# Kernel optimization log

Hardware: AMD Instinct MI355X
Metric: run time of the kernel (lower is better)

The kernel has to match this reference:

```python
import jax, jax.numpy as jnp
import numpy as np

N = 50000
E = 800000
IN_DIM = 128
HEADS = 4
OUT_DIM = 32
LEAKY_ALPHA = 0.4
BN_EPS = 1e-5


def setup_inputs() -> dict:
    key = jax.random.key(0)
    k_x, k_e, k_w, k_as, k_at = jax.random.split(key, 5)
    x = jax.random.normal(k_x, (N, IN_DIM), dtype=jnp.float32)
    edge_index = jax.random.randint(k_e, (2, E), 0, N, dtype=jnp.int32)
    # Linear weight stored as (in_dim, heads*out_dim) so that h = x @ W
    w_bound = 1.0 / np.sqrt(IN_DIM)
    W = jax.random.uniform(k_w, (IN_DIM, HEADS * OUT_DIM), dtype=jnp.float32,
                           minval=-w_bound, maxval=w_bound)
    # xavier_uniform with gain=1.414 on (heads, out_dim)
    xav = 1.414 * np.sqrt(6.0 / (HEADS + OUT_DIM))
    a_src = jax.random.uniform(k_as, (HEADS, OUT_DIM), dtype=jnp.float32, minval=-xav, maxval=xav)
    a_tgt = jax.random.uniform(k_at, (HEADS, OUT_DIM), dtype=jnp.float32, minval=-xav, maxval=xav)
    # BatchNorm affine params (fresh init: gamma=1, beta=0)
    gamma = jnp.ones((HEADS * OUT_DIM,), dtype=jnp.float32)
    beta = jnp.zeros((HEADS * OUT_DIM,), dtype=jnp.float32)
    return {"x": x, "W": W, "a_src": a_src, "a_tgt": a_tgt,
            "gamma": gamma, "beta": beta, "edge_index": edge_index}


def reference(x, W, a_src, a_tgt, gamma, beta, edge_index):
    src = edge_index[0]
    tgt = edge_index[1]
    n = x.shape[0]
    # Linear projection -> (N, H, D)
    h = (x @ W).reshape(n, HEADS, OUT_DIM)
    h_src = h[src]   # (E, H, D)
    h_tgt = h[tgt]   # (E, H, D)
    # Per-edge, per-head attention logits
    e_src = jnp.einsum('ehd,hd->eh', h_src, a_src)
    e_tgt = jnp.einsum('ehd,hd->eh', h_tgt, a_tgt)
    e = jax.nn.leaky_relu(e_src + e_tgt, negative_slope=LEAKY_ALPHA)
    # Global (per-head) max subtraction for numerical stability, as in original
    e = e - jnp.max(e, axis=0, keepdims=True)
    alpha = jnp.exp(e)  # (E, H)
    # Segment softmax denominator over target nodes
    alpha_sum = jax.ops.segment_sum(alpha, tgt, num_segments=n) + 1e-16  # (N, H)
    alpha = alpha / alpha_sum[tgt]
    # dropout is identity in eval mode
    # Weighted aggregation of source features into targets
    h_prime = h_src * alpha[:, :, None]  # (E, H, D)
    out = jax.ops.segment_sum(h_prime, tgt, num_segments=n)  # (N, H, D)
    out = out.reshape(n, HEADS * OUT_DIM)  # concat=True
    # BatchNorm1d in training mode: biased batch statistics
    mean = jnp.mean(out, axis=0)
    var = jnp.mean(jnp.square(out - mean), axis=0)
    out = (out - mean) * jax.lax.rsqrt(var + BN_EPS) * gamma + beta
    return out
```

## Files before the change

### kernel.cpp

```cpp
#include <hip/hip_runtime.h>
#include <math.h>

#define N_NODES 50000
#define E_EDGES 800000
#define IN_DIM 128
#define HEADS 4
#define OUT_DIM 32
#define HD 128
#define LEAKY 0.4f
#define BN_EPS 1e-5f

#define BSH 7
#define NB ((N_NODES + 127) >> BSH)
#define FB 196
#define FCH 4096
#define PCAP 2560
#define SRTCAP 3072
#define SCCH ((NB + 63) / 64)
#define K1B ((N_NODES + 63) / 64)
#define K2_BLOCKS 32
#define NPART 32

typedef __attribute__((ext_vector_type(8))) short short8;
typedef __attribute__((ext_vector_type(8))) unsigned short us8;
typedef __attribute__((ext_vector_type(4))) float f32x4;

__device__ __forceinline__ unsigned enc_max(float f) {
    unsigned u = __float_as_uint(f);
    return ((int)u >= 0) ? (u | 0x80000000u) : ~u;
}
__device__ __forceinline__ float dec_max(unsigned u) {
    return (u & 0x80000000u) ? __uint_as_float(u ^ 0x80000000u)
                             : __uint_as_float(~u);
}

__device__ __forceinline__ float leaky(float v) {
    return v > 0.f ? v : LEAKY * v;
}

__device__ __forceinline__ unsigned short f2bf(float f) {
    unsigned u = __float_as_uint(f);
    u = (u + 0x7FFFu + ((u >> 16) & 1u)) >> 16;
    return (unsigned short)u;
}
__device__ __forceinline__ float bf2f(unsigned short u) {
    return __uint_as_float(((unsigned)u) << 16);
}

struct FillSh { int est[FCH]; int hist[NB]; int rbase[NB]; };
union F1Sh { unsigned short Wl[32 * 64 * 8]; FillSh fl; };

__global__ __launch_bounds__(256) void f1_gemm_fill(
    const float* __restrict__ x, const float* __restrict__ W,
    const float* __restrict__ a_src, const float* __restrict__ a_tgt,
    const int* __restrict__ src, const int* __restrict__ tgt,
    int* __restrict__ bcur, int* __restrict__ ebkt,
    unsigned short* __restrict__ hb, float* __restrict__ s,
    float* __restrict__ t)
{
    __shared__ F1Sh sh;
    const int tid = threadIdx.x;

    if (blockIdx.x >= K1B) {
        int* est   = sh.fl.est;
        int* hist  = sh.fl.hist;
        int* rbase = sh.fl.rbase;
        int beg = (blockIdx.x - K1B) * FCH;
        int cnt = min(beg + FCH, E_EDGES) - beg;
        for (int i = tid; i < NB; i += 256) hist[i] = 0;
        __syncthreads();
        for (int j = tid; j < cnt; j += 256) {
            int sv = src[beg + j], tv = tgt[beg + j];
            est[j] = sv | (tv << 16);
            atomicAdd(&hist[tv >> BSH], 1);
        }
        __syncthreads();
        for (int i = tid; i < NB; i += 256) {
            int c = hist[i];
            if (c) {
                int r = atomicAdd(&bcur[i], c);
                rbase[i] = i * PCAP + min(r, PCAP);
            }
        }
        __syncthreads();
        for (int i = tid; i < NB; i += 256) hist[i] = 0;
        __syncthreads();
        for (int j = tid; j < cnt; j += 256) {
            int p  = est[j];
            int tv = (int)((unsigned)p >> 16);
            int b  = tv >> BSH;
            int off = atomicAdd(&hist[b], 1);
            int idx = rbase[b] + off;
            if (idx < (b + 1) * PCAP)
                ebkt[idx] = (p & 0xFFFF) | ((tv & 127) << 16);
        }
        return;
    }

    unsigned short* Wl = sh.Wl;
    for (int idx = tid; idx < 2048; idx += 256) {
        int l  = idx & 63;
        int f  = idx >> 6;
        int nt = f >> 2, kc = f & 3;
        int kbase = kc * 32 + ((l >> 4) << 3);
        int col   = nt * 16 + (l & 15);
        unsigned short* dst = &Wl[idx * 8];
#pragma unroll
        for (int j = 0; j < 8; j++)
            dst[j] = f2bf(W[(kbase + j) * HD + col]);
    }
    __syncthreads();

    const int wave = tid >> 6, lane = tid & 63;
    const int quad = lane >> 4, rl = lane & 15;
    const int row0 = blockIdx.x * 64 + wave * 16;
    const int crow = min(row0 + rl, N_NODES - 1);

    short8 a[4];
    const float* xp = x + (size_t)crow * IN_DIM + quad * 8;
#pragma unroll
    for (int kc = 0; kc < 4; kc++) {
        float4 v0 = *(const float4*)(xp + kc * 32);
        float4 v1 = *(const float4*)(xp + kc * 32 + 4);
        short8 av;
        av[0] = (short)f2bf(v0.x); av[1] = (short)f2bf(v0.y);
        av[2] = (short)f2bf(v0.z); av[3] = (short)f2bf(v0.w);
        av[4] = (short)f2bf(v1.x); av[5] = (short)f2bf(v1.y);
        av[6] = (short)f2bf(v1.z); av[7] = (short)f2bf(v1.w);
        a[kc] = av;
    }

    float asv[8], atv[8];
#pragma unroll
    for (int nt = 0; nt < 8; nt++) {
        asv[nt] = a_src[nt * 16 + rl];
        atv[nt] = a_tgt[nt * 16 + rl];
    }

    float ps[4][4], pt[4][4];
#pragma unroll
    for (int hh = 0; hh < 4; hh++)
#pragma unroll
        for (int r = 0; r < 4; r++) { ps[hh][r] = 0.f; pt[hh][r] = 0.f; }

#pragma unroll
    for (int nt = 0; nt < 8; nt++) {
        f32x4 acc = {0.f, 0.f, 0.f, 0.f};
#pragma unroll
        for (int kc = 0; kc < 4; kc++) {
            short8 b = *(const short8*)&Wl[((nt * 4 + kc) * 64 + lane) * 8];
            acc = __builtin_amdgcn_mfma_f32_16x16x32_bf16(a[kc], b, acc, 0, 0, 0);
        }
        const int ocol = nt * 16 + rl;
        const int hh   = nt >> 1;
#pragma unroll
        for (int r = 0; r < 4; r++) {
            int orow = row0 + quad * 4 + r;
            if (orow < N_NODES)
                hb[(size_t)orow * HD + ocol] = f2bf(acc[r]);
            ps[hh][r] = fmaf(acc[r], asv[nt], ps[hh][r]);
            pt[hh][r] = fmaf(acc[r], atv[nt], pt[hh][r]);
        }
    }

#pragma unroll
    for (int m = 1; m <= 8; m <<= 1) {
#pragma unroll
        for (int hh = 0; hh < 4; hh++)
#pragma unroll
            for (int r = 0; r < 4; r++) {
                ps[hh][r] += __shfl_xor(ps[hh][r], m, 64);
                pt[hh][r] += __shfl_xor(pt[hh][r], m, 64);
            }
    }
    if (rl == 0) {
#pragma unroll
        for (int r = 0; r < 4; r++) {
            int orow = row0 + quad * 4 + r;
            if (orow < N_NODES) {
#pragma unroll
                for (int hh = 0; hh < 4; hh++) {
                    s[orow * HEADS + hh] = ps[hh][r];
                    t[orow * HEADS + hh] = pt[hh][r];
                }
            }
        }
    }
}

struct SortSh {
    int ebl[SRTCAP]; int srt[SRTCAP]; int csc[NB + 1];
    int bins[128]; int deg_l[128]; int excl_l[128]; int cur_l[128];
    int wtot; int btot;
};
union F2Sh { SortSh so; float red[4][8]; };

__global__ __launch_bounds__(256) void f2_sort_max(
    const int* __restrict__ bcur, const int* __restrict__ ebkt,
    int* __restrict__ rowptr, unsigned short* __restrict__ esrc,
    const float* __restrict__ s, const float* __restrict__ t,
    unsigned* __restrict__ smax, unsigned* __restrict__ tmax)
{
    __shared__ F2Sh sh;
    int tid  = threadIdx.x;
    int lane = tid & 63, wv = tid >> 6;

    if (blockIdx.x >= NB) {
        int bI = blockIdx.x - NB;
        float sm0 = -INFINITY, sm1 = -INFINITY, sm2 = -INFINITY, sm3 = -INFINITY;
        float tm0 = -INFINITY, tm1 = -INFINITY, tm2 = -INFINITY, tm3 = -INFINITY;
        for (int n = bI * 256 + tid; n < N_NODES; n += K2_BLOCKS * 256) {
            float4 s4 = ((const float4*)s)[n];
            float4 t4 = ((const float4*)t)[n];
            sm0 = fmaxf(sm0, s4.x); sm1 = fmaxf(sm1, s4.y);
            sm2 = fmaxf(sm2, s4.z); sm3 = fmaxf(sm3, s4.w);
            tm0 = fmaxf(tm0, t4.x); tm1 = fmaxf(tm1, t4.y);
            tm2 = fmaxf(tm2, t4.z); tm3 = fmaxf(tm3, t4.w);
        }
#pragma unroll
        for (int m = 32; m >= 1; m >>= 1) {
            sm0 = fmaxf(sm0, __shfl_xor(sm0, m, 64));
            sm1 = fmaxf(sm1, __shfl_xor(sm1, m, 64));
            sm2 = fmaxf(sm2, __shfl_xor(sm2, m, 64));
            sm3 = fmaxf(sm3, __shfl_xor(sm3, m, 64));
            tm0 = fmaxf(tm0, __shfl_xor(tm0, m, 64));
            tm1 = fmaxf(tm1, __shfl_xor(tm1, m, 64));
            tm2 = fmaxf(tm2, __shfl_xor(tm2, m, 64));
            tm3 = fmaxf(tm3, __shfl_xor(tm3, m, 64));
        }
        if (lane == 0) {
            sh.red[wv][0] = sm0; sh.red[wv][1] = sm1;
            sh.red[wv][2] = sm2; sh.red[wv][3] = sm3;
            sh.red[wv][4] = tm0; sh.red[wv][5] = tm1;
            sh.red[wv][6] = tm2; sh.red[wv][7] = tm3;
        }
        __syncthreads();
        if (tid < 8) {
            float v = fmaxf(fmaxf(sh.red[0][tid], sh.red[1][tid]),
                            fmaxf(sh.red[2][tid], sh.red[3][tid]));
            unsigned* dst = (tid < 4) ? &smax[tid] : &tmax[tid - 4];
            atomicMax(dst, enc_max(v));
        }
        return;
    }

    int b = blockIdx.x;
    int* ebl    = sh.so.ebl;
    int* srt    = sh.so.srt;
    int* csc    = sh.so.csc;
    int* bins   = sh.so.bins;
    int* deg_l  = sh.so.deg_l;
    int* excl_l = sh.so.excl_l;
    int* cur_l  = sh.so.cur_l;

    for (int i = tid; i < NB; i += 256) csc[i] = min(bcur[i], PCAP);
    if (tid < 128) { deg_l[tid] = 0; cur_l[tid] = 0; bins[tid] = 0; }
    __syncthreads();
    if (tid < 64) {
        int cb = tid * SCCH;
        int loc[SCCH];
        int sum = 0;
#pragma unroll
        for (int k = 0; k < SCCH; k++) {
            int idx = cb + k;
            int v = (idx < NB) ? csc[idx] : 0;
            loc[k] = sum; sum += v;
        }
        int ss = sum;
#pragma unroll
        for (int off = 1; off < 64; off <<= 1) {
            int u = __shfl_up(ss, off, 64);
            if (tid >= off) ss += u;
        }
        int excl = ss - sum;
#pragma unroll
        for (int k = 0; k < SCCH; k++) {
            int idx = cb + k;
            if (idx < NB) csc[idx] = excl + loc[k];
        }
        if (tid == 63) {
            csc[NB] = excl + sum;
            if (b == 0) rowptr[N_NODES] = excl + sum;
        }
    }
    __syncthreads();
    int base_in = b * PCAP;
    int base    = csc[b];
    int cnt     = csc[b + 1] - base;

    for (int j = tid; j < cnt; j += 256) {
        int p = ebkt[base_in + j];
        ebl[j] = p;
        atomicAdd(&bins[(p & 0xFFFF) >> 9], 1);
    }
    __syncthreads();
    {
        int v = (tid < 128) ? bins[tid] : 0;
        int ssv = v;
#pragma unroll
        for (int off = 1; off < 64; off <<= 1) {
            int u = __shfl_up(ssv, off, 64);
            if (lane >= off) ssv += u;
        }
        if (tid == 63) sh.so.btot = ssv;
        __syncthreads();
        if (tid < 128) bins[tid] = ssv - v + ((wv == 1) ? sh.so.btot : 0);
        __syncthreads();
    }
    for (int j = tid; j < cnt; j += 256) {
        int p = ebl[j];
        int pos = atomicAdd(&bins[(p & 0xFFFF) >> 9], 1);
        srt[pos] = p;
    }
    __syncthreads();
    for (int j = tid; j < cnt; j += 256)
        atomicAdd(&deg_l[srt[j] >> 16], 1);
    __syncthreads();

    int v = (tid < 128) ? deg_l[tid] : 0;
    int sv2 = v;
#pragma unroll
    for (int off = 1; off < 64; off <<= 1) {
        int u = __shfl_up(sv2, off, 64);
        if (lane >= off) sv2 += u;
    }
    if (tid == 63) sh.so.wtot = sv2;
    __syncthreads();
    if (tid < 128) {
        int ex = sv2 - v + ((wv == 1) ? sh.so.wtot : 0);
        excl_l[tid] = ex;
        int node = (b << BSH) + tid;
        if (node < N_NODES) rowptr[node] = base + ex;
    }
    __syncthreads();
    for (int j = tid; j < cnt; j += 256) {
        int p  = srt[j];
        int tl = p >> 16;
        int off = atomicAdd(&cur_l[tl], 1);
        esrc[base + excl_l[tl] + off] = (unsigned short)(p & 0xFFFF);
    }
}

__global__ __launch_bounds__(256) void f3_pull_stats(
    const int* __restrict__ rowptr, const unsigned short* __restrict__ esrc,
    const float* __restrict__ s, const float* __restrict__ t,
    const unsigned* __restrict__ smax, const unsigned* __restrict__ tmax,
    const unsigned short* __restrict__ hb, unsigned short* __restrict__ outpb,
    float* __restrict__ bnsum_part, float* __restrict__ bnsq_part)
{
    __shared__ float lsum[HD], lsq[HD];
    int tid = threadIdx.x;
    if (tid < HD) { lsum[tid] = 0.f; lsq[tid] = 0.f; }
    __syncthreads();

    int g = blockIdx.x * 256 + tid;
    int node = g >> 4;
    int lane = g & 15;
    int head = lane >> 2;
    int beg = rowptr[node];
    int end = rowptr[node + 1];
    float mx = leaky(dec_max(smax[head]) + dec_max(tmax[head]));
    float tv = t[node * HEADS + head];

    float p0 = 0.f, p1 = 0.f, p2 = 0.f, p3 = 0.f;
    float p4 = 0.f, p5 = 0.f, p6 = 0.f, p7 = 0.f, psum = 0.f;
    float q0 = 0.f, q1 = 0.f, q2 = 0.f, q3 = 0.f;
    float q4 = 0.f, q5 = 0.f, q6 = 0.f, q7 = 0.f, qsum = 0.f;
    const unsigned short* hbase = hb + lane * 8;

    for (int j = beg; j < end; j += 8) {
        int lim = end - j;
        int si[8];
#pragma unroll
        for (int u = 0; u < 8; u++) {
            int uu = (u < lim) ? u : (lim - 1);
            si[u] = esrc[j + uu];
        }
        float sv[8];
        us8 hv[8];
#pragma unroll
        for (int u = 0; u < 8; u++) {
            sv[u] = s[si[u] * HEADS + head];
            hv[u] = *(const us8*)(hbase + (size_t)si[u] * HD);
        }
        float al[8];
#pragma unroll
        for (int u = 0; u < 8; u++) {
            float a = __expf(leaky(sv[u] + tv) - mx);
            al[u] = (u < lim) ? a : 0.f;
        }
#pragma unroll
        for (int u = 0; u < 8; u += 2) {
            float a0 = al[u], a1 = al[u + 1];
            p0 = fmaf(a0, bf2f(hv[u][0]), p0);  q0 = fmaf(a1, bf2f(hv[u+1][0]), q0);
            p1 = fmaf(a0, bf2f(hv[u][1]), p1);  q1 = fmaf(a1, bf2f(hv[u+1][1]), q1);
            p2 = fmaf(a0, bf2f(hv[u][2]), p2);  q2 = fmaf(a1, bf2f(hv[u+1][2]), q2);
            p3 = fmaf(a0, bf2f(hv[u][3]), p3);  q3 = fmaf(a1, bf2f(hv[u+1][3]), q3);
            p4 = fmaf(a0, bf2f(hv[u][4]), p4);  q4 = fmaf(a1, bf2f(hv[u+1][4]), q4);
            p5 = fmaf(a0, bf2f(hv[u][5]), p5);  q5 = fmaf(a1, bf2f(hv[u+1][5]), q5);
            p6 = fmaf(a0, bf2f(hv[u][6]), p6);  q6 = fmaf(a1, bf2f(hv[u+1][6]), q6);
            p7 = fmaf(a0, bf2f(hv[u][7]), p7);  q7 = fmaf(a1, bf2f(hv[u+1][7]), q7);
            psum += a0; qsum += a1;
        }
    }

    float w = 1.0f / (psum + qsum + 1e-16f);
    us8 o;
    o[0] = f2bf((p0 + q0) * w); o[1] = f2bf((p1 + q1) * w);
    o[2] = f2bf((p2 + q2) * w); o[3] = f2bf((p3 + q3) * w);
    o[4] = f2bf((p4 + q4) * w); o[5] = f2bf((p5 + q5) * w);
    o[6] = f2bf((p6 + q6) * w); o[7] = f2bf((p7 + q7) * w);
    *(us8*)(outpb + (size_t)node * HD + lane * 8) = o;

#pragma unroll
    for (int i = 0; i < 8; i++) {
        float f = bf2f(o[i]);
        atomicAdd(&lsum[lane * 8 + i], f);
        atomicAdd(&lsq[lane * 8 + i], f * f);
    }
    __syncthreads();
    if (tid < HD) {
        int ps = blockIdx.x & (NPART - 1);
        unsafeAtomicAdd(&bnsum_part[ps * HD + tid], lsum[tid]);
        unsafeAtomicAdd(&bnsq_part [ps * HD + tid], lsq[tid]);
    }
}

__global__ __launch_bounds__(256) void f4_apply(
    const unsigned short* __restrict__ outpb,
    const float* __restrict__ bnsum_part, const float* __restrict__ bnsq_part,
    const float* __restrict__ gamma, const float* __restrict__ beta,
    float* __restrict__ out)
{
    __shared__ float scs[HD], shs[HD];
    int tid = threadIdx.x;
    if (tid < HD) {
        float sm = 0.f, sq = 0.f;
#pragma unroll 4
        for (int p = 0; p < NPART; p++) {
            sm += bnsum_part[p * HD + tid];
            sq += bnsq_part [p * HD + tid];
        }
        float inv_n = 1.0f / (float)N_NODES;
        float mean = sm * inv_n;
        float var  = sq * inv_n - mean * mean;
        float sc   = gamma[tid] * rsqrtf(var + BN_EPS);
        scs[tid] = sc;
        shs[tid] = beta[tid] - mean * sc;
    }
    __syncthreads();

    int c8  = tid & 15;
    int grp = tid >> 4;
    float scale[8], shift[8];
#pragma unroll
    for (int i = 0; i < 8; i++) {
        scale[i] = scs[c8 * 8 + i];
        shift[i] = shs[c8 * 8 + i];
    }
    int base = blockIdx.x * 256;
    int end  = min(base + 256, N_NODES);
    for (int r = base + grp; r < end; r += 16) {
        us8 v = *(const us8*)(outpb + (size_t)r * HD + c8 * 8);
        float4 o0, o1;
        o0.x = fmaf(bf2f(v[0]), scale[0], shift[0]);
        o0.y = fmaf(bf2f(v[1]), scale[1], shift[1]);
        o0.z = fmaf(bf2f(v[2]), scale[2], shift[2]);
        o0.w = fmaf(bf2f(v[3]), scale[3], shift[3]);
        o1.x = fmaf(bf2f(v[4]), scale[4], shift[4]);
        o1.y = fmaf(bf2f(v[5]), scale[5], shift[5]);
        o1.z = fmaf(bf2f(v[6]), scale[6], shift[6]);
        o1.w = fmaf(bf2f(v[7]), scale[7], shift[7]);
        float* op = out + (size_t)r * HD + c8 * 8;
        ((float4*)op)[0] = o0;
        ((float4*)op)[1] = o1;
    }
}

extern "C" void kernel_launch(void* const* d_in, const int* in_sizes, int n_in,
                              void* d_out, int out_size, void* d_ws, size_t ws_size,
                              hipStream_t stream)
{
    const float* x     = (const float*)d_in[0];
    const float* W     = (const float*)d_in[1];
    const float* a_src = (const float*)d_in[2];
    const float* a_tgt = (const float*)d_in[3];
    const float* gamma = (const float*)d_in[4];
    const float* beta  = (const float*)d_in[5];
    const int*   eidx  = (const int*)d_in[6];
    const int* src = eidx;
    const int* tgt = eidx + E_EDGES;
    float* out = (float*)d_out;

    unsigned short* hb    = (unsigned short*)d_ws;
    float*          s     = (float*)d_ws + 3200000;
    float*          t     = s + (size_t)N_NODES * HEADS;
    unsigned short* outpb = (unsigned short*)(t + (size_t)N_NODES * HEADS);
    int*            ebkt  = (int*)outpb;
    unsigned short* esrc  = outpb + 6400000;
    int*            rowptr= (int*)(esrc + E_EDGES);
    int*      bcur  = rowptr + N_NODES + 1;
    unsigned* smax  = (unsigned*)(bcur + 392);
    unsigned* tmax  = smax + 4;
    float*    bnsum_part = (float*)(tmax + 4);
    float*    bnsq_part  = bnsum_part + NPART * HD;
    size_t zero_bytes = (392 + 8 + 2 * NPART * HD) * 4;
    hipMemsetAsync(bcur, 0, zero_bytes, stream);

    f1_gemm_fill<<<K1B + FB, 256, 0, stream>>>(x, W, a_src, a_tgt,
                                               src, tgt, bcur, ebkt,
                                               hb, s, t);
    f2_sort_max<<<NB + K2_BLOCKS, 256, 0, stream>>>(bcur, ebkt, rowptr, esrc,
                                                    s, t, smax, tmax);
    f3_pull_stats<<<(N_NODES * 16) / 256, 256, 0, stream>>>(
        rowptr, esrc, s, t, smax, tmax, hb, outpb, bnsum_part, bnsq_part);
    f4_apply<<<(N_NODES + 255) / 256, 256, 0, stream>>>(
        outpb, bnsum_part, bnsq_part, gamma, beta, out);
}
```

Measured before the change: 219.9 us.

## Fuse four kernels into one persistent kernel with software grid barriers

Merges the GEMM/bucket-fill, sort/max, pull-aggregation and BatchNorm stages into a single kernel of K1B+FB blocks separated by atomic-counter grid barriers. The goal is to remove three kernel-launch gaps and their tail effects. The sort step drops the secondary source-binning pass, and BN statistics are now gathered in a separate stage over contiguous row ranges. Correctness depends on all 978 blocks being co-resident, which launch_bounds(256,4) on 256 CUs should allow. The aggregation loop becomes grid-strided, and each barrier adds spin-wait latency.

```diff
diff --git a/kernel.cpp b/kernel.cpp
--- a/kernel.cpp
+++ b/kernel.cpp
@@ -15,11 +15,12 @@
 #define FB 196
 #define FCH 4096
 #define PCAP 2560
-#define SRTCAP 3072
 #define SCCH ((NB + 63) / 64)
 #define K1B ((N_NODES + 63) / 64)
 #define K2_BLOCKS 32
-#define NPART 32
+#define GRID (K1B + FB)
+#define NPART 64
+#define SROWS ((N_NODES + GRID - 1) / GRID)
 
 typedef __attribute__((ext_vector_type(8))) short short8;
 typedef __attribute__((ext_vector_type(8))) unsigned short us8;
@@ -47,25 +48,53 @@
     return __uint_as_float(((unsigned)u) << 16);
 }
 
+__device__ __forceinline__ void gridbar(int* ctr) {
+    __syncthreads();
+    if (threadIdx.x == 0) {
+        __hip_atomic_fetch_add(ctr, 1, __ATOMIC_ACQ_REL,
+                               __HIP_MEMORY_SCOPE_AGENT);
+        while (__hip_atomic_load(ctr, __ATOMIC_ACQUIRE,
+                                 __HIP_MEMORY_SCOPE_AGENT) < GRID)
+            __builtin_amdgcn_s_sleep(8);
+    }
+    __syncthreads();
+}
+
 struct FillSh { int est[FCH]; int hist[NB]; int rbase[NB]; };
-union F1Sh { unsigned short Wl[32 * 64 * 8]; FillSh fl; };
-
-__global__ __launch_bounds__(256) void f1_gemm_fill(
+struct SortSh {
+    int ebl[PCAP]; int csc[NB + 1];
+    int deg_l[128]; int excl_l[128]; int cur_l[128];
+    int wtot;
+};
+struct StatSh { float lsum[HD]; float lsq[HD]; };
+union MegaSh { unsigned short Wl[32 * 64 * 8]; FillSh fl; SortSh so;
+               StatSh st; float red[4][8]; };
+
+__global__ __launch_bounds__(256, 4) void mega(
     const float* __restrict__ x, const float* __restrict__ W,
     const float* __restrict__ a_src, const float* __restrict__ a_tgt,
     const int* __restrict__ src, const int* __restrict__ tgt,
     int* __restrict__ bcur, int* __restrict__ ebkt,
     unsigned short* __restrict__ hb, float* __restrict__ s,
-    float* __restrict__ t)
+    float* __restrict__ t, int* __restrict__ rowptr,
+    unsigned short* __restrict__ esrc,
+    unsigned* __restrict__ smax, unsigned* __restrict__ tmax,
+    unsigned short* __restrict__ outpb,
+    float* __restrict__ bnp_sum, float* __restrict__ bnp_sq,
+    float* __restrict__ gsc, float* __restrict__ gsh,
+    const float* __restrict__ gamma, const float* __restrict__ beta,
+    float* __restrict__ out, int* __restrict__ bars)
 {
-    __shared__ F1Sh sh;
-    const int tid = threadIdx.x;
-
-    if (blockIdx.x >= K1B) {
+    __shared__ MegaSh sh;
+    const int tid  = threadIdx.x;
+    const int bid  = blockIdx.x;
+    const int lane = tid & 63, wv = tid >> 6;
+
+    if (bid >= K1B) {
         int* est   = sh.fl.est;
         int* hist  = sh.fl.hist;
         int* rbase = sh.fl.rbase;
-        int beg = (blockIdx.x - K1B) * FCH;
+        int beg = (bid - K1B) * FCH;
         int cnt = min(beg + FCH, E_EDGES) - beg;
         for (int i = tid; i < NB; i += 256) hist[i] = 0;
         __syncthreads();
@@ -94,119 +123,173 @@
             if (idx < (b + 1) * PCAP)
                 ebkt[idx] = (p & 0xFFFF) | ((tv & 127) << 16);
         }
-        return;
-    }
-
-    unsigned short* Wl = sh.Wl;
-    for (int idx = tid; idx < 2048; idx += 256) {
-        int l  = idx & 63;
-        int f  = idx >> 6;
-        int nt = f >> 2, kc = f & 3;
-        int kbase = kc * 32 + ((l >> 4) << 3);
-        int col   = nt * 16 + (l & 15);
-        unsigned short* dst = &Wl[idx * 8];
-#pragma unroll
-        for (int j = 0; j < 8; j++)
-            dst[j] = f2bf(W[(kbase + j) * HD + col]);
-    }
-    __syncthreads();
-
-    const int wave = tid >> 6, lane = tid & 63;
-    const int quad = lane >> 4, rl = lane & 15;
-    const int row0 = blockIdx.x * 64 + wave * 16;
-    const int crow = min(row0 + rl, N_NODES - 1);
-
-    short8 a[4];
-    const float* xp = x + (size_t)crow * IN_DIM + quad * 8;
-#pragma unroll
-    for (int kc = 0; kc < 4; kc++) {
-        float4 v0 = *(const float4*)(xp + kc * 32);
-        float4 v1 = *(const float4*)(xp + kc * 32 + 4);
-        short8 av;
-        av[0] = (short)f2bf(v0.x); av[1] = (short)f2bf(v0.y);
-        av[2] = (short)f2bf(v0.z); av[3] = (short)f2bf(v0.w);
-        av[4] = (short)f2bf(v1.x); av[5] = (short)f2bf(v1.y);
-        av[6] = (short)f2bf(v1.z); av[7] = (short)f2bf(v1.w);
-        a[kc] = av;
-    }
-
-    float asv[8], atv[8];
-#pragma unroll
-    for (int nt = 0; nt < 8; nt++) {
-        asv[nt] = a_src[nt * 16 + rl];
-        atv[nt] = a_tgt[nt * 16 + rl];
-    }
-
-    float ps[4][4], pt[4][4];
-#pragma unroll
-    for (int hh = 0; hh < 4; hh++)
-#pragma unroll
-        for (int r = 0; r < 4; r++) { ps[hh][r] = 0.f; pt[hh][r] = 0.f; }
-
-#pragma unroll
-    for (int nt = 0; nt < 8; nt++) {
-        f32x4 acc = {0.f, 0.f, 0.f, 0.f};
+    } else {
+        unsigned short* Wl = sh.Wl;
+        for (int idx = tid; idx < 2048; idx += 256) {
+            int l  = idx & 63;
+            int f  = idx >> 6;
+            int nt = f >> 2, kc = f & 3;
+            int kbase = kc * 32 + ((l >> 4) << 3);
+            int col   = nt * 16 + (l & 15);
+            unsigned short* dst = &Wl[idx * 8];
+#pragma unroll
+            for (int j = 0; j < 8; j++)
+                dst[j] = f2bf(W[(kbase + j) * HD + col]);
+        }
+        __syncthreads();
+
+        const int quad = lane >> 4, rl = lane & 15;
+        const int row0 = bid * 64 + wv * 16;
+        const int crow = min(row0 + rl, N_NODES - 1);
+
+        short8 a[4];
+        const float* xp = x + (size_t)crow * IN_DIM + quad * 8;
 #pragma unroll
         for (int kc = 0; kc < 4; kc++) {
-            short8 b = *(const short8*)&Wl[((nt * 4 + kc) * 64 + lane) * 8];
-            acc = __builtin_amdgcn_mfma_f32_16x16x32_bf16(a[kc], b, acc, 0, 0, 0);
-        }
-        const int ocol = nt * 16 + rl;
-        const int hh   = nt >> 1;
-#pragma unroll
-        for (int r = 0; r < 4; r++) {
-            int orow = row0 + quad * 4 + r;
-            if (orow < N_NODES)
-                hb[(size_t)orow * HD + ocol] = f2bf(acc[r]);
-            ps[hh][r] = fmaf(acc[r], asv[nt], ps[hh][r]);
-            pt[hh][r] = fmaf(acc[r], atv[nt], pt[hh][r]);
-        }
-    }
-
-#pragma unroll
-    for (int m = 1; m <= 8; m <<= 1) {
+            float4 v0 = *(const float4*)(xp + kc * 32);
+            float4 v1 = *(const float4*)(xp + kc * 32 + 4);
+            short8 av;
+            av[0] = (short)f2bf(v0.x); av[1] = (short)f2bf(v0.y);
+            av[2] = (short)f2bf(v0.z); av[3] = (short)f2bf(v0.w);
+            av[4] = (short)f2bf(v1.x); av[5] = (short)f2bf(v1.y);
+            av[6] = (short)f2bf(v1.z); av[7] = (short)f2bf(v1.w);
+            a[kc] = av;
+        }
+
+        float asv[8], atv[8];
+#pragma unroll
+        for (int nt = 0; nt < 8; nt++) {
+            asv[nt] = a_src[nt * 16 + rl];
+            atv[nt] = a_tgt[nt * 16 + rl];
+        }
+
+        float ps[4][4], pt[4][4];
 #pragma unroll
         for (int hh = 0; hh < 4; hh++)
 #pragma unroll
+            for (int r = 0; r < 4; r++) { ps[hh][r] = 0.f; pt[hh][r] = 0.f; }
+
+#pragma unroll
+        for (int nt = 0; nt < 8; nt++) {
+            f32x4 acc = {0.f, 0.f, 0.f, 0.f};
+#pragma unroll
+            for (int kc = 0; kc < 4; kc++) {
+                short8 b = *(const short8*)&Wl[((nt * 4 + kc) * 64 + lane) * 8];
+                acc = __builtin_amdgcn_mfma_f32_16x16x32_bf16(a[kc], b, acc, 0, 0, 0);
+            }
+            const int ocol = nt * 16 + rl;
+            const int hh   = nt >> 1;
+#pragma unroll
             for (int r = 0; r < 4; r++) {
-                ps[hh][r] += __shfl_xor(ps[hh][r], m, 64);
-                pt[hh][r] += __shfl_xor(pt[hh][r], m, 64);
-            }
-    }
-    if (rl == 0) {
-#pragma unroll
-        for (int r = 0; r < 4; r++) {
-            int orow = row0 + quad * 4 + r;
-            if (orow < N_NODES) {
-#pragma unroll
-                for (int hh = 0; hh < 4; hh++) {
-                    s[orow * HEADS + hh] = ps[hh][r];
-                    t[orow * HEADS + hh] = pt[hh][r];
+                int orow = row0 + quad * 4 + r;
+                if (orow < N_NODES)
+                    hb[(size_t)orow * HD + ocol] = f2bf(acc[r]);
+                ps[hh][r] = fmaf(acc[r], asv[nt], ps[hh][r]);
+                pt[hh][r] = fmaf(acc[r], atv[nt], pt[hh][r]);
+            }
+        }
+
+#pragma unroll
+        for (int m = 1; m <= 8; m <<= 1) {
+#pragma unroll
+            for (int hh = 0; hh < 4; hh++)
+#pragma unroll
+                for (int r = 0; r < 4; r++) {
+                    ps[hh][r] += __shfl_xor(ps[hh][r], m, 64);
+                    pt[hh][r] += __shfl_xor(pt[hh][r], m, 64);
                 }
-            }
-        }
-    }
-}
-
-struct SortSh {
-    int ebl[SRTCAP]; int srt[SRTCAP]; int csc[NB + 1];
-    int bins[128]; int deg_l[128]; int excl_l[128]; int cur_l[128];
-    int wtot; int btot;
-};
-union F2Sh { SortSh so; float red[4][8]; };
-
-__global__ __launch_bounds__(256) void f2_sort_max(
-    const int* __restrict__ bcur, const int* __restrict__ ebkt,
-    int* __restrict__ rowptr, unsigned short* __restrict__ esrc,
-    const float* __restrict__ s, const float* __restrict__ t,
-    unsigned* __restrict__ smax, unsigned* __restrict__ tmax)
-{
-    __shared__ F2Sh sh;
-    int tid  = threadIdx.x;
-    int lane = tid & 63, wv = tid >> 6;
-
-    if (blockIdx.x >= NB) {
-        int bI = blockIdx.x - NB;
+        }
+        if (rl == 0) {
+#pragma unroll
+            for (int r = 0; r < 4; r++) {
+                int orow = row0 + quad * 4 + r;
+                if (orow < N_NODES) {
+#pragma unroll
+                    for (int hh = 0; hh < 4; hh++) {
+                        s[orow * HEADS + hh] = ps[hh][r];
+                        t[orow * HEADS + hh] = pt[hh][r];
+                    }
+                }
+            }
+        }
+    }
+
+    gridbar(&bars[0]);
+
+    if (bid < NB) {
+        int b = bid;
+        int* ebl    = sh.so.ebl;
+        int* csc    = sh.so.csc;
+        int* deg_l  = sh.so.deg_l;
+        int* excl_l = sh.so.excl_l;
+        int* cur_l  = sh.so.cur_l;
+
+        for (int i = tid; i < NB; i += 256) csc[i] = min(bcur[i], PCAP);
+        if (tid < 128) { deg_l[tid] = 0; cur_l[tid] = 0; }
+        __syncthreads();
+        if (tid < 64) {
+            int cb = tid * SCCH;
+            int loc[SCCH];
+            int sum = 0;
+#pragma unroll
+            for (int k = 0; k < SCCH; k++) {
+                int idx = cb + k;
+                int v = (idx < NB) ? csc[idx] : 0;
+                loc[k] = sum; sum += v;
+            }
+            int ss = sum;
+#pragma unroll
+            for (int off = 1; off < 64; off <<= 1) {
+                int u = __shfl_up(ss, off, 64);
+                if (tid >= off) ss += u;
+            }
+            int excl = ss - sum;
+#pragma unroll
+            for (int k = 0; k < SCCH; k++) {
+                int idx = cb + k;
+                if (idx < NB) csc[idx] = excl + loc[k];
+            }
+            if (tid == 63) {
+                csc[NB] = excl + sum;
+                if (b == 0) rowptr[N_NODES] = excl + sum;
+            }
+        }
+        __syncthreads();
+        int base_in = b * PCAP;
+        int base    = csc[b];
+        int cnt     = csc[b + 1] - base;
+
+        for (int j = tid; j < cnt; j += 256) {
+            int p = ebkt[base_in + j];
+            ebl[j] = p;
+            atomicAdd(&deg_l[p >> 16], 1);
+        }
+        __syncthreads();
+
+        int v = (tid < 128) ? deg_l[tid] : 0;
+        int sv2 = v;
+#pragma unroll
+        for (int off = 1; off < 64; off <<= 1) {
+            int u = __shfl_up(sv2, off, 64);
+            if (lane >= off) sv2 += u;
+        }
+        if (tid == 63) sh.so.wtot = sv2;
+        __syncthreads();
+        if (tid < 128) {
+            int ex = sv2 - v + ((wv == 1) ? sh.so.wtot : 0);
+            excl_l[tid] = ex;
+            int node = (b << BSH) + tid;
+            if (node < N_NODES) rowptr[node] = base + ex;
+        }
+        __syncthreads();
+        for (int j = tid; j < cnt; j += 256) {
+            int p  = ebl[j];
+            int tl = p >> 16;
+            int off = atomicAdd(&cur_l[tl], 1);
+            esrc[base + excl_l[tl] + off] = (unsigned short)(p & 0xFFFF);
+        }
+    } else if (bid < NB + K2_BLOCKS) {
+        int bI = bid - NB;
         float sm0 = -INFINITY, sm1 = -INFINITY, sm2 = -INFINITY, sm3 = -INFINITY;
         float tm0 = -INFINITY, tm1 = -INFINITY, tm2 = -INFINITY, tm3 = -INFINITY;
         for (int n = bI * 256 + tid; n < N_NODES; n += K2_BLOCKS * 256) {
@@ -241,239 +324,149 @@
             unsigned* dst = (tid < 4) ? &smax[tid] : &tmax[tid - 4];
             atomicMax(dst, enc_max(v));
         }
-        return;
-    }
-
-    int b = blockIdx.x;
-    int* ebl    = sh.so.ebl;
-    int* srt    = sh.so.srt;
-    int* csc    = sh.so.csc;
-    int* bins   = sh.so.bins;
-    int* deg_l  = sh.so.deg_l;
-    int* excl_l = sh.so.excl_l;
-    int* cur_l  = sh.so.cur_l;
-
-    for (int i = tid; i < NB; i += 256) csc[i] = min(bcur[i], PCAP);
-    if (tid < 128) { deg_l[tid] = 0; cur_l[tid] = 0; bins[tid] = 0; }
-    __syncthreads();
-    if (tid < 64) {
-        int cb = tid * SCCH;
-        int loc[SCCH];
-        int sum = 0;
-#pragma unroll
-        for (int k = 0; k < SCCH; k++) {
-            int idx = cb + k;
-            int v = (idx < NB) ? csc[idx] : 0;
-            loc[k] = sum; sum += v;
-        }
-        int ss = sum;
-#pragma unroll
-        for (int off = 1; off < 64; off <<= 1) {
-            int u = __shfl_up(ss, off, 64);
-            if (tid >= off) ss += u;
-        }
-        int excl = ss - sum;
-#pragma unroll
-        for (int k = 0; k < SCCH; k++) {
-            int idx = cb + k;
-            if (idx < NB) csc[idx] = excl + loc[k];
-        }
-        if (tid == 63) {
-            csc[NB] = excl + sum;
-            if (b == 0) rowptr[N_NODES] = excl + sum;
-        }
-    }
-    __syncthreads();
-    int base_in = b * PCAP;
-    int base    = csc[b];
-    int cnt     = csc[b + 1] - base;
-
-    for (int j = tid; j < cnt; j += 256) {
-        int p = ebkt[base_in + j];
-        ebl[j] = p;
-        atomicAdd(&bins[(p & 0xFFFF) >> 9], 1);
-    }
-    __syncthreads();
+    }
+
+    gridbar(&bars[1]);
+
+    for (int g = bid * 256 + tid; g < N_NODES * 16; g += GRID * 256) {
+        int node = g >> 4;
+        int lane16 = g & 15;
+        int head = lane16 >> 2;
+        int beg = rowptr[node];
+        int end = rowptr[node + 1];
+        float mx = leaky(dec_max(smax[head]) + dec_max(tmax[head]));
+        float tv = t[node * HEADS + head];
+
+        float p0 = 0.f, p1 = 0.f, p2 = 0.f, p3 = 0.f;
+        float p4 = 0.f, p5 = 0.f, p6 = 0.f, p7 = 0.f, psum = 0.f;
+        float q0 = 0.f, q1 = 0.f, q2 = 0.f, q3 = 0.f;
+        float q4 = 0.f, q5 = 0.f, q6 = 0.f, q7 = 0.f, qsum = 0.f;
+        const unsigned short* hbase = hb + lane16 * 8;
+
+        for (int j = beg; j < end; j += 8) {
+            int lim = end - j;
+            int si[8];
+#pragma unroll
+            for (int u = 0; u < 8; u++) {
+                int uu = (u < lim) ? u : (lim - 1);
+                si[u] = __builtin_nontemporal_load(&esrc[j + uu]);
+            }
+            float sv[8];
+            us8 hv[8];
+#pragma unroll
+            for (int u = 0; u < 8; u++) {
+                sv[u] = s[si[u] * HEADS + head];
+                hv[u] = *(const us8*)(hbase + (size_t)si[u] * HD);
+            }
+            float al[8];
+#pragma unroll
+            for (int u = 0; u < 8; u++) {
+                float a = __expf(leaky(sv[u] + tv) - mx);
+                al[u] = (u < lim) ? a : 0.f;
+            }
+#pragma unroll
+            for (int u = 0; u < 8; u += 2) {
+                float a0 = al[u], a1 = al[u + 1];
+                p0 = fmaf(a0, bf2f(hv[u][0]), p0);  q0 = fmaf(a1, bf2f(hv[u+1][0]), q0);
+                p1 = fmaf(a0, bf2f(hv[u][1]), p1);  q1 = fmaf(a1, bf2f(hv[u+1][1]), q1);
+                p2 = fmaf(a0, bf2f(hv[u][2]), p2);  q2 = fmaf(a1, bf2f(hv[u+1][2]), q2);
+                p3 = fmaf(a0, bf2f(hv[u][3]), p3);  q3 = fmaf(a1, bf2f(hv[u+1][3]), q3);
+                p4 = fmaf(a0, bf2f(hv[u][4]), p4);  q4 = fmaf(a1, bf2f(hv[u+1][4]), q4);
+                p5 = fmaf(a0, bf2f(hv[u][5]), p5);  q5 = fmaf(a1, bf2f(hv[u+1][5]), q5);
+                p6 = fmaf(a0, bf2f(hv[u][6]), p6);  q6 = fmaf(a1, bf2f(hv[u+1][6]), q6);
+                p7 = fmaf(a0, bf2f(hv[u][7]), p7);  q7 = fmaf(a1, bf2f(hv[u+1][7]), q7);
+                psum += a0; qsum += a1;
+            }
+        }
+
+        float w = 1.0f / (psum + qsum + 1e-16f);
+        us8 o;
+        o[0] = f2bf((p0 + q0) * w); o[1] = f2bf((p1 + q1) * w);
+        o[2] = f2bf((p2 + q2) * w); o[3] = f2bf((p3 + q3) * w);
+        o[4] = f2bf((p4 + q4) * w); o[5] = f2bf((p5 + q5) * w);
+        o[6] = f2bf((p6 + q6) * w); o[7] = f2bf((p7 + q7) * w);
+        *(us8*)(outpb + (size_t)node * HD + lane16 * 8) = o;
+    }
+
+    gridbar(&bars[2]);
+
     {
-        int v = (tid < 128) ? bins[tid] : 0;
-        int ssv = v;
-#pragma unroll
-        for (int off = 1; off < 64; off <<= 1) {
-            int u = __shfl_up(ssv, off, 64);
-            if (lane >= off) ssv += u;
-        }
-        if (tid == 63) sh.so.btot = ssv;
-        __syncthreads();
-        if (tid < 128) bins[tid] = ssv - v + ((wv == 1) ? sh.so.btot : 0);
-        __syncthreads();
-    }
-    for (int j = tid; j < cnt; j += 256) {
-        int p = ebl[j];
-        int pos = atomicAdd(&bins[(p & 0xFFFF) >> 9], 1);
-        srt[pos] = p;
-    }
-    __syncthreads();
-    for (int j = tid; j < cnt; j += 256)
-        atomicAdd(&deg_l[srt[j] >> 16], 1);
-    __syncthreads();
-
-    int v = (tid < 128) ? deg_l[tid] : 0;
-    int sv2 = v;
-#pragma unroll
-    for (int off = 1; off < 64; off <<= 1) {
-        int u = __shfl_up(sv2, off, 64);
-        if (lane >= off) sv2 += u;
-    }
-    if (tid == 63) sh.so.wtot = sv2;
-    __syncthreads();
-    if (tid < 128) {
-        int ex = sv2 - v + ((wv == 1) ? sh.so.wtot : 0);
-        excl_l[tid] = ex;
-        int node = (b << BSH) + tid;
-        if (node < N_NODES) rowptr[node] = base + ex;
-    }
-    __syncthreads();
-    for (int j = tid; j < cnt; j += 256) {
-        int p  = srt[j];
-        int tl = p >> 16;
-        int off = atomicAdd(&cur_l[tl], 1);
-        esrc[base + excl_l[tl] + off] = (unsigned short)(p & 0xFFFF);
-    }
-}
-
-__global__ __launch_bounds__(256) void f3_pull_stats(
-    const int* __restrict__ rowptr, const unsigned short* __restrict__ esrc,
-    const float* __restrict__ s, const float* __restrict__ t,
-    const unsigned* __restrict__ smax, const unsigned* __restrict__ tmax,
-    const unsigned short* __restrict__ hb, unsigned short* __restrict__ outpb,
-    float* __restrict__ bnsum_part, float* __restrict__ bnsq_part)
-{
-    __shared__ float lsum[HD], lsq[HD];
-    int tid = threadIdx.x;
-    if (tid < HD) { lsum[tid] = 0.f; lsq[tid] = 0.f; }
-    __syncthreads();
-
-    int g = blockIdx.x * 256 + tid;
-    int node = g >> 4;
-    int lane = g & 15;
-    int head = lane >> 2;
-    int beg = rowptr[node];
-    int end = rowptr[node + 1];
-    float mx = leaky(dec_max(smax[head]) + dec_max(tmax[head]));
-    float tv = t[node * HEADS + head];
-
-    float p0 = 0.f, p1 = 0.f, p2 = 0.f, p3 = 0.f;
-    float p4 = 0.f, p5 = 0.f, p6 = 0.f, p7 = 0.f, psum = 0.f;
-    float q0 = 0.f, q1 = 0.f, q2 = 0.f, q3 = 0.f;
-    float q4 = 0.f, q5 = 0.f, q6 = 0.f, q7 = 0.f, qsum = 0.f;
-    const unsigned short* hbase = hb + lane * 8;
-
-    for (int j = beg; j < end; j += 8) {
-        int lim = end - j;
-        int si[8];
-#pragma unroll
-        for (int u = 0; u < 8; u++) {
-            int uu = (u < lim) ? u : (lim - 1);
-            si[u] = esrc[j + uu];
-        }
-        float sv[8];
-        us8 hv[8];
-#pragma unroll
-        for (int u = 0; u < 8; u++) {
-            sv[u] = s[si[u] * HEADS + head];
-            hv[u] = *(const us8*)(hbase + (size_t)si[u] * HD);
-        }
-        float al[8];
-#pragma unroll
-        for (int u = 0; u < 8; u++) {
-            float a = __expf(leaky(sv[u] + tv) - mx);
-            al[u] = (u < lim) ? a : 0.f;
-        }
-#pragma unroll
-        for (int u = 0; u < 8; u += 2) {
-            float a0 = al[u], a1 = al[u + 1];
-            p0 = fmaf(a0, bf2f(hv[u][0]), p0);  q0 = fmaf(a1, bf2f(hv[u+1][0]), q0);
-            p1 = fmaf(a0, bf2f(hv[u][1]), p1);  q1 = fmaf(a1, bf2f(hv[u+1][1]), q1);
-            p2 = fmaf(a0, bf2f(hv[u][2]), p2);  q2 = fmaf(a1, bf2f(hv[u+1][2]), q2);
-            p3 = fmaf(a0, bf2f(hv[u][3]), p3);  q3 = fmaf(a1, bf2f(hv[u+1][3]), q3);
-            p4 = fmaf(a0, bf2f(hv[u][4]), p4);  q4 = fmaf(a1, bf2f(hv[u+1][4]), q4);
-            p5 = fmaf(a0, bf2f(hv[u][5]), p5);  q5 = fmaf(a1, bf2f(hv[u+1][5]), q5);
-            p6 = fmaf(a0, bf2f(hv[u][6]), p6);  q6 = fmaf(a1, bf2f(hv[u+1][6]), q6);
-            p7 = fmaf(a0, bf2f(hv[u][7]), p7);  q7 = fmaf(a1, bf2f(hv[u+1][7]), q7);
-            psum += a0; qsum += a1;
-        }
-    }
-
-    float w = 1.0f / (psum + qsum + 1e-16f);
-    us8 o;
-    o[0] = f2bf((p0 + q0) * w); o[1] = f2bf((p1 + q1) * w);
-    o[2] = f2bf((p2 + q2) * w); o[3] = f2bf((p3 + q3) * w);
-    o[4] = f2bf((p4 + q4) * w); o[5] = f2bf((p5 + q5) * w);
-    o[6] = f2bf((p6 + q6) * w); o[7] = f2bf((p7 + q7) * w);
-    *(us8*)(outpb + (size_t)node * HD + lane * 8) = o;
-
-#pragma unroll
-    for (int i = 0; i < 8; i++) {
-        float f = bf2f(o[i]);
-        atomicAdd(&lsum[lane * 8 + i], f);
-        atomicAdd(&lsq[lane * 8 + i], f * f);
-    }
-    __syncthreads();
-    if (tid < HD) {
-        int ps = blockIdx.x & (NPART - 1);
-        unsafeAtomicAdd(&bnsum_part[ps * HD + tid], lsum[tid]);
-        unsafeAtomicAdd(&bnsq_part [ps * HD + tid], lsq[tid]);
-    }
-}
-
-__global__ __launch_bounds__(256) void f4_apply(
-    const unsigned short* __restrict__ outpb,
-    const float* __restrict__ bnsum_part, const float* __restrict__ bnsq_part,
-    const float* __restrict__ gamma, const float* __restrict__ beta,
-    float* __restrict__ out)
-{
-    __shared__ float scs[HD], shs[HD];
-    int tid = threadIdx.x;
-    if (tid < HD) {
+        int c8  = tid & 15;
+        int grp = tid >> 4;
+        if (tid < HD) { sh.st.lsum[tid] = 0.f; sh.st.lsq[tid] = 0.f; }
+        __syncthreads();
+        int rbeg = bid * SROWS;
+        int rend = min(rbeg + SROWS, N_NODES);
+        float sm[8], sq[8];
+#pragma unroll
+        for (int i = 0; i < 8; i++) { sm[i] = 0.f; sq[i] = 0.f; }
+        for (int r = rbeg + grp; r < rend; r += 16) {
+            us8 v = *(const us8*)(outpb + (size_t)r * HD + c8 * 8);
+#pragma unroll
+            for (int i = 0; i < 8; i++) {
+                float f = bf2f(v[i]);
+                sm[i] += f;
+                sq[i] = fmaf(f, f, sq[i]);
+            }
+        }
+#pragma unroll
+        for (int i = 0; i < 8; i++) {
+            atomicAdd(&sh.st.lsum[c8 * 8 + i], sm[i]);
+            atomicAdd(&sh.st.lsq[c8 * 8 + i], sq[i]);
+        }
+        __syncthreads();
+        if (tid < HD && rbeg < N_NODES) {
+            int ps = bid & (NPART - 1);
+            unsafeAtomicAdd(&bnp_sum[ps * HD + tid], sh.st.lsum[tid]);
+            unsafeAtomicAdd(&bnp_sq [ps * HD + tid], sh.st.lsq[tid]);
+        }
+    }
+
+    gridbar(&bars[3]);
+
+    if (bid == 0 && tid < HD) {
         float sm = 0.f, sq = 0.f;
 #pragma unroll 4
         for (int p = 0; p < NPART; p++) {
-            sm += bnsum_part[p * HD + tid];
-            sq += bnsq_part [p * HD + tid];
+            sm += bnp_sum[p * HD + tid];
+            sq += bnp_sq [p * HD + tid];
         }
         float inv_n = 1.0f / (float)N_NODES;
         float mean = sm * inv_n;
         float var  = sq * inv_n - mean * mean;
         float sc   = gamma[tid] * rsqrtf(var + BN_EPS);
-        scs[tid] = sc;
-        shs[tid] = beta[tid] - mean * sc;
-    }
-    __syncthreads();
-
-    int c8  = tid & 15;
-    int grp = tid >> 4;
-    float scale[8], shift[8];
-#pragma unroll
-    for (int i = 0; i < 8; i++) {
-        scale[i] = scs[c8 * 8 + i];
-        shift[i] = shs[c8 * 8 + i];
-    }
-    int base = blockIdx.x * 256;
-    int end  = min(base + 256, N_NODES);
-    for (int r = base + grp; r < end; r += 16) {
-        us8 v = *(const us8*)(outpb + (size_t)r * HD + c8 * 8);
-        float4 o0, o1;
-        o0.x = fmaf(bf2f(v[0]), scale[0], shift[0]);
-        o0.y = fmaf(bf2f(v[1]), scale[1], shift[1]);
-        o0.z = fmaf(bf2f(v[2]), scale[2], shift[2]);
-        o0.w = fmaf(bf2f(v[3]), scale[3], shift[3]);
-        o1.x = fmaf(bf2f(v[4]), scale[4], shift[4]);
-        o1.y = fmaf(bf2f(v[5]), scale[5], shift[5]);
-        o1.z = fmaf(bf2f(v[6]), scale[6], shift[6]);
-        o1.w = fmaf(bf2f(v[7]), scale[7], shift[7]);
-        float* op = out + (size_t)r * HD + c8 * 8;
-        ((float4*)op)[0] = o0;
-        ((float4*)op)[1] = o1;
+        gsc[tid] = sc;
+        gsh[tid] = beta[tid] - mean * sc;
+    }
+
+    gridbar(&bars[4]);
+
+    {
+        int c8  = tid & 15;
+        int grp = tid >> 4;
+        float scale[8], shift[8];
+#pragma unroll
+        for (int i = 0; i < 8; i++) {
+            scale[i] = gsc[c8 * 8 + i];
+            shift[i] = gsh[c8 * 8 + i];
+        }
+        int rbeg = bid * SROWS;
+        int rend = min(rbeg + SROWS, N_NODES);
+        for (int r = rbeg + grp; r < rend; r += 16) {
+            us8 v = *(const us8*)(outpb + (size_t)r * HD + c8 * 8);
+            float4 o0, o1;
+            o0.x = fmaf(bf2f(v[0]), scale[0], shift[0]);
+            o0.y = fmaf(bf2f(v[1]), scale[1], shift[1]);
+            o0.z = fmaf(bf2f(v[2]), scale[2], shift[2]);
+            o0.w = fmaf(bf2f(v[3]), scale[3], shift[3]);
+            o1.x = fmaf(bf2f(v[4]), scale[4], shift[4]);
+            o1.y = fmaf(bf2f(v[5]), scale[5], shift[5]);
+            o1.z = fmaf(bf2f(v[6]), scale[6], shift[6]);
+            o1.w = fmaf(bf2f(v[7]), scale[7], shift[7]);
+            float* op = out + (size_t)r * HD + c8 * 8;
+            ((float4*)op)[0] = o0;
+            ((float4*)op)[1] = o1;
+        }
     }
 }
 
@@ -502,18 +495,16 @@
     int*      bcur  = rowptr + N_NODES + 1;
     unsigned* smax  = (unsigned*)(bcur + 392);
     unsigned* tmax  = smax + 4;
-    float*    bnsum_part = (float*)(tmax + 4);
-    float*    bnsq_part  = bnsum_part + NPART * HD;
-    size_t zero_bytes = (392 + 8 + 2 * NPART * HD) * 4;
+    int*      bars  = (int*)(tmax + 4);
+    float*    bnp_sum = (float*)(bars + 8);
+    float*    bnp_sq  = bnp_sum + NPART * HD;
+    size_t zero_bytes = (392 + 8 + 8 + 2 * NPART * HD) * 4;
+    float*    gsc = bnp_sq + NPART * HD;
+    float*    gsh = gsc + HD;
     hipMemsetAsync(bcur, 0, zero_bytes, stream);
 
-    f1_gemm_fill<<<K1B + FB, 256, 0, stream>>>(x, W, a_src, a_tgt,
-                                               src, tgt, bcur, ebkt,
-                                               hb, s, t);
-    f2_sort_max<<<NB + K2_BLOCKS, 256, 0, stream>>>(bcur, ebkt, rowptr, esrc,
-                                                    s, t, smax, tmax);
-    f3_pull_stats<<<(N_NODES * 16) / 256, 256, 0, stream>>>(
-        rowptr, esrc, s, t, smax, tmax, hb, outpb, bnsum_part, bnsq_part);
-    f4_apply<<<(N_NODES + 255) / 256, 256, 0, stream>>>(
-        outpb, bnsum_part, bnsq_part, gamma, beta, out);
-}
+    mega<<<GRID, 256, 0, stream>>>(x, W, a_src, a_tgt, src, tgt,
+                                   bcur, ebkt, hb, s, t, rowptr, esrc,
+                                   smax, tmax, outpb, bnp_sum, bnp_sq,
+                                   gsc, gsh, gamma, beta, out, bars);
+}
```

New measurement: 857.5 us. +290.0%, slower.

## Drop source-bin presort in bucket sort and use wave-shuffle BN partial reduction

Applied to the files above, without the earlier changes.

Removes the intermediate counting sort by source-id bins inside the per-bucket CSR build, counting degrees and scattering directly from the loaded edge list, which cuts shared memory and several barriers. In the pull kernel, the shared-memory atomic BatchNorm reduction and block barrier are replaced with xor-shuffle reductions within each wave followed by global atomics from 16 lanes. The partial-sum count is doubled to spread atomic contention, and edge source indices are read with nontemporal loads. The drop of the source presort loses source locality within each target's edge list, which may hurt gather cache behaviour, and per-wave global atomics increase atomic traffic.

```diff
diff --git a/kernel.cpp b/kernel.cpp
--- a/kernel.cpp
+++ b/kernel.cpp
@@ -15,11 +15,10 @@
 #define FB 196
 #define FCH 4096
 #define PCAP 2560
-#define SRTCAP 3072
 #define SCCH ((NB + 63) / 64)
 #define K1B ((N_NODES + 63) / 64)
 #define K2_BLOCKS 32
-#define NPART 32
+#define NPART 64
 
 typedef __attribute__((ext_vector_type(8))) short short8;
 typedef __attribute__((ext_vector_type(8))) unsigned short us8;
@@ -189,9 +188,9 @@
 }
 
 struct SortSh {
-    int ebl[SRTCAP]; int srt[SRTCAP]; int csc[NB + 1];
-    int bins[128]; int deg_l[128]; int excl_l[128]; int cur_l[128];
-    int wtot; int btot;
+    int ebl[PCAP]; int csc[NB + 1];
+    int deg_l[128]; int excl_l[128]; int cur_l[128];
+    int wtot;
 };
 union F2Sh { SortSh so; float red[4][8]; };
 
@@ -246,15 +245,13 @@
 
     int b = blockIdx.x;
     int* ebl    = sh.so.ebl;
-    int* srt    = sh.so.srt;
     int* csc    = sh.so.csc;
-    int* bins   = sh.so.bins;
     int* deg_l  = sh.so.deg_l;
     int* excl_l = sh.so.excl_l;
     int* cur_l  = sh.so.cur_l;
 
     for (int i = tid; i < NB; i += 256) csc[i] = min(bcur[i], PCAP);
-    if (tid < 128) { deg_l[tid] = 0; cur_l[tid] = 0; bins[tid] = 0; }
+    if (tid < 128) { deg_l[tid] = 0; cur_l[tid] = 0; }
     __syncthreads();
     if (tid < 64) {
         int cb = tid * SCCH;
@@ -291,30 +288,8 @@
     for (int j = tid; j < cnt; j += 256) {
         int p = ebkt[base_in + j];
         ebl[j] = p;
-        atomicAdd(&bins[(p & 0xFFFF) >> 9], 1);
-    }
-    __syncthreads();
-    {
-        int v = (tid < 128) ? bins[tid] : 0;
-        int ssv = v;
-#pragma unroll
-        for (int off = 1; off < 64; off <<= 1) {
-            int u = __shfl_up(ssv, off, 64);
-            if (lane >= off) ssv += u;
-        }
-        if (tid == 63) sh.so.btot = ssv;
-        __syncthreads();
-        if (tid < 128) bins[tid] = ssv - v + ((wv == 1) ? sh.so.btot : 0);
-        __syncthreads();
-    }
-    for (int j = tid; j < cnt; j += 256) {
-        int p = ebl[j];
-        int pos = atomicAdd(&bins[(p & 0xFFFF) >> 9], 1);
-        srt[pos] = p;
-    }
-    __syncthreads();
-    for (int j = tid; j < cnt; j += 256)
-        atomicAdd(&deg_l[srt[j] >> 16], 1);
+        atomicAdd(&deg_l[p >> 16], 1);
+    }
     __syncthreads();
 
     int v = (tid < 128) ? deg_l[tid] : 0;
@@ -334,26 +309,21 @@
     }
     __syncthreads();
     for (int j = tid; j < cnt; j += 256) {
-        int p  = srt[j];
+        int p  = ebl[j];
         int tl = p >> 16;
         int off = atomicAdd(&cur_l[tl], 1);
         esrc[base + excl_l[tl] + off] = (unsigned short)(p & 0xFFFF);
     }
 }
 
-__global__ __launch_bounds__(256) void f3_pull_stats(
+__global__ __launch_bounds__(256) void k4_pull(
     const int* __restrict__ rowptr, const unsigned short* __restrict__ esrc,
     const float* __restrict__ s, const float* __restrict__ t,
     const unsigned* __restrict__ smax, const unsigned* __restrict__ tmax,
     const unsigned short* __restrict__ hb, unsigned short* __restrict__ outpb,
-    float* __restrict__ bnsum_part, float* __restrict__ bnsq_part)
+    float* __restrict__ bnp_sum, float* __restrict__ bnp_sq)
 {
-    __shared__ float lsum[HD], lsq[HD];
-    int tid = threadIdx.x;
-    if (tid < HD) { lsum[tid] = 0.f; lsq[tid] = 0.f; }
-    __syncthreads();
-
-    int g = blockIdx.x * 256 + tid;
+    int g = blockIdx.x * 256 + threadIdx.x;
     int node = g >> 4;
     int lane = g & 15;
     int head = lane >> 2;
@@ -374,7 +344,7 @@
 #pragma unroll
         for (int u = 0; u < 8; u++) {
             int uu = (u < lim) ? u : (lim - 1);
-            si[u] = esrc[j + uu];
+            si[u] = __builtin_nontemporal_load(&esrc[j + uu]);
         }
         float sv[8];
         us8 hv[8];
@@ -412,23 +382,35 @@
     o[6] = f2bf((p6 + q6) * w); o[7] = f2bf((p7 + q7) * w);
     *(us8*)(outpb + (size_t)node * HD + lane * 8) = o;
 
+    float sm[8], sq[8];
 #pragma unroll
     for (int i = 0; i < 8; i++) {
         float f = bf2f(o[i]);
-        atomicAdd(&lsum[lane * 8 + i], f);
-        atomicAdd(&lsq[lane * 8 + i], f * f);
-    }
-    __syncthreads();
-    if (tid < HD) {
+        sm[i] = f;
+        sq[i] = f * f;
+    }
+#pragma unroll
+    for (int i = 0; i < 8; i++) {
+        sm[i] += __shfl_xor(sm[i], 16, 64);
+        sq[i] += __shfl_xor(sq[i], 16, 64);
+        sm[i] += __shfl_xor(sm[i], 32, 64);
+        sq[i] += __shfl_xor(sq[i], 32, 64);
+    }
+    if ((threadIdx.x & 63) < 16) {
         int ps = blockIdx.x & (NPART - 1);
-        unsafeAtomicAdd(&bnsum_part[ps * HD + tid], lsum[tid]);
-        unsafeAtomicAdd(&bnsq_part [ps * HD + tid], lsq[tid]);
-    }
-}
-
-__global__ __launch_bounds__(256) void f4_apply(
+        float* bs = bnp_sum + ps * HD + lane * 8;
+        float* bq = bnp_sq  + ps * HD + lane * 8;
+#pragma unroll
+        for (int i = 0; i < 8; i++) {
+            unsafeAtomicAdd(&bs[i], sm[i]);
+            unsafeAtomicAdd(&bq[i], sq[i]);
+        }
+    }
+}
+
+__global__ __launch_bounds__(256) void k6_apply(
     const unsigned short* __restrict__ outpb,
-    const float* __restrict__ bnsum_part, const float* __restrict__ bnsq_part,
+    const float* __restrict__ bnp_sum, const float* __restrict__ bnp_sq,
     const float* __restrict__ gamma, const float* __restrict__ beta,
     float* __restrict__ out)
 {
@@ -438,8 +420,8 @@
         float sm = 0.f, sq = 0.f;
 #pragma unroll 4
         for (int p = 0; p < NPART; p++) {
-            sm += bnsum_part[p * HD + tid];
-            sq += bnsq_part [p * HD + tid];
+            sm += bnp_sum[p * HD + tid];
+            sq += bnp_sq [p * HD + tid];
         }
         float inv_n = 1.0f / (float)N_NODES;
         float mean = sm * inv_n;
@@ -502,8 +484,8 @@
     int*      bcur  = rowptr + N_NODES + 1;
     unsigned* smax  = (unsigned*)(bcur + 392);
     unsigned* tmax  = smax + 4;
-    float*    bnsum_part = (float*)(tmax + 4);
-    float*    bnsq_part  = bnsum_part + NPART * HD;
+    float*    bnp_sum = (float*)(tmax + 4);
+    float*    bnp_sq  = bnp_sum + NPART * HD;
     size_t zero_bytes = (392 + 8 + 2 * NPART * HD) * 4;
     hipMemsetAsync(bcur, 0, zero_bytes, stream);
 
@@ -512,8 +494,8 @@
                                                hb, s, t);
     f2_sort_max<<<NB + K2_BLOCKS, 256, 0, stream>>>(bcur, ebkt, rowptr, esrc,
                                                     s, t, smax, tmax);
-    f3_pull_stats<<<(N_NODES * 16) / 256, 256, 0, stream>>>(
-        rowptr, esrc, s, t, smax, tmax, hb, outpb, bnsum_part, bnsq_part);
-    f4_apply<<<(N_NODES + 255) / 256, 256, 0, stream>>>(
-        outpb, bnsum_part, bnsq_part, gamma, beta, out);
-}
+    k4_pull<<<(N_NODES * 16) / 256, 256, 0, stream>>>(
+        rowptr, esrc, s, t, smax, tmax, hb, outpb, bnp_sum, bnp_sq);
+    k6_apply<<<(N_NODES + 255) / 256, 256, 0, stream>>>(
+        outpb, bnp_sum, bnp_sq, gamma, beta, out);
+}
```

Result: slower. 265.9 us (+20.9%).
